# Optimization experiments

Hardware: AMD Instinct MI355X
Metric: run time of the kernel (lower is better)

Reference implementation:

```python
import jax, jax.numpy as jnp
import numpy as np

N_NODES = 50000
N_EDGES = 800000
D = 64


def setup_inputs() -> dict:
    key = jax.random.key(0)
    ks = jax.random.split(key, 8)
    feats = jax.random.normal(ks[0], (N_NODES, D), dtype=jnp.float32)
    src = jax.random.randint(ks[1], (N_EDGES,), 0, N_NODES, dtype=jnp.int32)
    dst = jax.random.randint(ks[2], (N_EDGES,), 0, N_NODES, dtype=jnp.int32)
    s = 1.0 / np.sqrt(D)
    return {
        "features": feats,
        "src": src,
        "dst": dst,
        "W_self1": jax.random.normal(ks[3], (D, D), dtype=jnp.float32) * s,
        "W_neigh1": jax.random.normal(ks[4], (D, D), dtype=jnp.float32) * s,
        "b1": jnp.zeros((D,), dtype=jnp.float32),
        "W_self2": jax.random.normal(ks[5], (D, D), dtype=jnp.float32) * s,
        "W_neigh2": jax.random.normal(ks[6], (D, D), dtype=jnp.float32) * s,
        "b2": jnp.zeros((D,), dtype=jnp.float32),
    }


def _sage_mean(feat, src, dst, W_self, W_neigh, b):
    # mean-aggregate neighbor features: sum over incoming edges / clamp(in_deg, 1)
    msg_sum = jax.ops.segment_sum(feat[src], dst, num_segments=N_NODES)
    deg = jax.ops.segment_sum(jnp.ones(src.shape, feat.dtype), dst, num_segments=N_NODES)
    h_neigh = msg_sum / jnp.maximum(deg, 1.0)[:, None]
    return feat @ W_self + h_neigh @ W_neigh + b


def reference(features, src, dst, W_self1, W_neigh1, b1, W_self2, W_neigh2, b2):
    x = jax.nn.relu(_sage_mean(features, src, dst, W_self1, W_neigh1, b1))
    x = jax.nn.relu(_sage_mean(x, src, dst, W_self2, W_neigh2, b2))
    # DotProductPredictor: u_dot_v per edge, sigmoid; forward applies sigmoid again
    edge_dot = jnp.sum(x[src] * x[dst], axis=-1)  # [E]
    return jax.nn.sigmoid(jax.nn.sigmoid(edge_dot))
```

## Files before the change

kernel.cpp:

```cpp
#include <hip/hip_runtime.h>
#include <math.h>

#define N_NODES 50000
#define N_EDGES 800000
#define D 64
#define CAP 48
#define NPART 8
#define PART_N (N_NODES / NPART)
#define ACHUNK 2048
#define NBLK_A ((N_EDGES + ACHUNK - 1) / ACHUNK)
#define SEG_CAP 448
#define NB_PER_PART 32

#define FB_OFF   0
#define HB_OFF   6400000
#define STG_OFF  12800000
#define CNTG_OFF 18432000
#define POS_OFF  19200000
#define BKT_OFF  19400704

__device__ __forceinline__ unsigned int bf_rtn(float x) {
    unsigned int b = __float_as_uint(x);
    return (b + 0x7fffu + ((b >> 16) & 1u)) >> 16;
}
__device__ __forceinline__ unsigned int bf2_pack(float lo, float hi) {
    return bf_rtn(lo) | (bf_rtn(hi) << 16);
}
__device__ __forceinline__ float4 bf4_unpack(uint2 q) {
    float4 r;
    r.x = __uint_as_float(q.x << 16);
    r.y = __uint_as_float(q.x & 0xffff0000u);
    r.z = __uint_as_float(q.y << 16);
    r.w = __uint_as_float(q.y & 0xffff0000u);
    return r;
}

__global__ void convert_feats_kernel(const float4* __restrict__ in, uint2* __restrict__ out,
                                     int* __restrict__ pos) {
    int i = blockIdx.x * blockDim.x + threadIdx.x;
    if (i < N_NODES) pos[i] = 0;
    float4 v = in[i];
    uint2 q;
    q.x = bf2_pack(v.x, v.y);
    q.y = bf2_pack(v.z, v.w);
    out[i] = q;
}

__global__ __launch_bounds__(256) void partition_edges_kernel(
    const int* __restrict__ src, const int* __restrict__ dst,
    unsigned int* __restrict__ stage, int* __restrict__ cntg) {
    __shared__ int cnt[NPART];
    const int tid = threadIdx.x;
    if (tid < NPART) cnt[tid] = 0;
    __syncthreads();

    const int base = blockIdx.x * ACHUNK;
    unsigned int* bstage = stage + blockIdx.x * (NPART * SEG_CAP);
#pragma unroll
    for (int j = 0; j < ACHUNK / 256; ++j) {
        int i = base + j * 256 + tid;
        if (i < N_EDGES) {
            int d = dst[i];
            int s = src[i];
            int p = d / PART_N;
            unsigned int val = ((unsigned int)(d - p * PART_N) << 16) | (unsigned int)s;
            int slot = atomicAdd(&cnt[p], 1);
            if (slot < SEG_CAP) bstage[p * SEG_CAP + slot] = val;
        }
    }
    __syncthreads();
    if (tid < NPART) cntg[blockIdx.x * NPART + tid] = cnt[tid];
}

__global__ __launch_bounds__(256) void scatter_bucket_kernel(
    const unsigned int* __restrict__ stage, const int* __restrict__ cntg,
    int* __restrict__ pos, int* __restrict__ bucket) {
    const int p = blockIdx.x & (NPART - 1);
    const int j = blockIdx.x >> 3;
    const int lo = p * PART_N;
    const int tid = threadIdx.x;
    for (int b = j; b < NBLK_A; b += NB_PER_PART) {
        const int c = cntg[b * NPART + p];
        const unsigned int* seg = stage + (b * NPART + p) * SEG_CAP;
        for (int i = tid; i < c; i += 256) {
            unsigned int v = seg[i];
            int d = lo + (int)(v >> 16);
            int s = (int)(v & 0xffffu);
            int slot = atomicAdd(&pos[d], 1);
            if (slot < CAP) bucket[d * CAP + slot] = s;
        }
    }
}

__global__ __launch_bounds__(256) void gather_mean_kernel(
    const uint2* __restrict__ xb,
    const int* __restrict__ pos,
    const int* __restrict__ bucket,
    uint2* __restrict__ h_out) {
    const int tid = threadIdx.x;
    const int lane = tid & 63;
    const int g = lane >> 4;
    const int sub = lane & 15;
    const int node = blockIdx.x * 16 + (tid >> 6) * 4 + g;

    const int deg = pos[node];
    const int cnt = (deg < CAP) ? deg : CAP;
    const int* brow = bucket + node * CAP;

#define ACC4(A, R) { A.x += R.x; A.y += R.y; A.z += R.z; A.w += R.w; }
    float4 a0 = make_float4(0.f, 0.f, 0.f, 0.f);
    float4 a1 = make_float4(0.f, 0.f, 0.f, 0.f);
    float4 a2 = make_float4(0.f, 0.f, 0.f, 0.f);
    float4 a3 = make_float4(0.f, 0.f, 0.f, 0.f);
    float4 a4 = make_float4(0.f, 0.f, 0.f, 0.f);
    float4 a5 = make_float4(0.f, 0.f, 0.f, 0.f);
    float4 a6 = make_float4(0.f, 0.f, 0.f, 0.f);
    float4 a7 = make_float4(0.f, 0.f, 0.f, 0.f);
    int j = 0;
    for (; j + 8 <= cnt; j += 8) {
        int4 i0 = *(const int4*)(brow + j);
        int4 i1 = *(const int4*)(brow + j + 4);
        float4 r0 = bf4_unpack(xb[i0.x * 16 + sub]);
        float4 r1 = bf4_unpack(xb[i0.y * 16 + sub]);
        float4 r2 = bf4_unpack(xb[i0.z * 16 + sub]);
        float4 r3 = bf4_unpack(xb[i0.w * 16 + sub]);
        float4 r4 = bf4_unpack(xb[i1.x * 16 + sub]);
        float4 r5 = bf4_unpack(xb[i1.y * 16 + sub]);
        float4 r6 = bf4_unpack(xb[i1.z * 16 + sub]);
        float4 r7 = bf4_unpack(xb[i1.w * 16 + sub]);
        ACC4(a0, r0); ACC4(a1, r1); ACC4(a2, r2); ACC4(a3, r3);
        ACC4(a4, r4); ACC4(a5, r5); ACC4(a6, r6); ACC4(a7, r7);
    }
    if (j + 4 <= cnt) {
        int4 i0 = *(const int4*)(brow + j);
        float4 r0 = bf4_unpack(xb[i0.x * 16 + sub]);
        float4 r1 = bf4_unpack(xb[i0.y * 16 + sub]);
        float4 r2 = bf4_unpack(xb[i0.z * 16 + sub]);
        float4 r3 = bf4_unpack(xb[i0.w * 16 + sub]);
        ACC4(a4, r0); ACC4(a5, r1); ACC4(a6, r2); ACC4(a7, r3);
        j += 4;
    }
    for (; j < cnt; ++j) {
        float4 r = bf4_unpack(xb[brow[j] * 16 + sub]);
        ACC4(a0, r);
    }
#undef ACC4
    float4 acc;
    acc.x = ((a0.x + a1.x) + (a2.x + a3.x)) + ((a4.x + a5.x) + (a6.x + a7.x));
    acc.y = ((a0.y + a1.y) + (a2.y + a3.y)) + ((a4.y + a5.y) + (a6.y + a7.y));
    acc.z = ((a0.z + a1.z) + (a2.z + a3.z)) + ((a4.z + a5.z) + (a6.z + a7.z));
    acc.w = ((a0.w + a1.w) + (a2.w + a3.w)) + ((a4.w + a5.w) + (a6.w + a7.w));
    float inv = 1.0f / fmaxf((float)deg, 1.0f);
    uint2 q;
    q.x = bf2_pack(acc.x * inv, acc.y * inv);
    q.y = bf2_pack(acc.z * inv, acc.w * inv);
    h_out[node * 16 + sub] = q;
}

__global__ __launch_bounds__(64, 3) void sage_gemm_kernel(
    const uint2* xb_self,
    const uint2* hb_in,
    const float* __restrict__ W_self, const float* __restrict__ W_neigh,
    const float* __restrict__ bias,
    uint2* x_out) {
    const int lane = threadIdx.x;
    const int g = lane >> 4;
    const int sub = lane & 15;
    const int nb = blockIdx.x * 16;

    const int n0 = nb + 0 * 4 + g;
    const int n1 = nb + 1 * 4 + g;
    const int n2 = nb + 2 * 4 + g;
    const int n3 = nb + 3 * 4 + g;
    const uint2* arow0 = xb_self + n0 * 16;
    const uint2* arow1 = xb_self + n1 * 16;
    const uint2* arow2 = xb_self + n2 * 16;
    const uint2* arow3 = xb_self + n3 * 16;
    const uint2* hrow0 = hb_in + n0 * 16;
    const uint2* hrow1 = hb_in + n1 * 16;
    const uint2* hrow2 = hb_in + n2 * 16;
    const uint2* hrow3 = hb_in + n3 * 16;

    const float4* Wsg = (const float4*)W_self;
    const float4* Wng = (const float4*)W_neigh;
    const float4 b4 = ((const float4*)bias)[sub];
    float4 accs0 = b4, accs1 = b4, accs2 = b4, accs3 = b4;

#pragma unroll 4
    for (int kk = 0; kk < 16; ++kk) {
        float4 ws0 = Wsg[(kk * 4 + 0) * 16 + sub];
        float4 ws1 = Wsg[(kk * 4 + 1) * 16 + sub];
        float4 ws2 = Wsg[(kk * 4 + 2) * 16 + sub];
        float4 ws3 = Wsg[(kk * 4 + 3) * 16 + sub];
        float4 wn0 = Wng[(kk * 4 + 0) * 16 + sub];
        float4 wn1 = Wng[(kk * 4 + 1) * 16 + sub];
        float4 wn2 = Wng[(kk * 4 + 2) * 16 + sub];
        float4 wn3 = Wng[(kk * 4 + 3) * 16 + sub];

#define SAGE_FMA(ACC, AROW, HROW)                                               \
        {                                                                       \
            float4 a4 = bf4_unpack((AROW)[kk]);                                 \
            float4 h4v = bf4_unpack((HROW)[kk]);                                \
            ACC.x += a4.x * ws0.x + a4.y * ws1.x + a4.z * ws2.x + a4.w * ws3.x  \
                   + h4v.x * wn0.x + h4v.y * wn1.x + h4v.z * wn2.x + h4v.w * wn3.x; \
            ACC.y += a4.x * ws0.y + a4.y * ws1.y + a4.z * ws2.y + a4.w * ws3.y  \
                   + h4v.x * wn0.y + h4v.y * wn1.y + h4v.z * wn2.y + h4v.w * wn3.y; \
            ACC.z += a4.x * ws0.z + a4.y * ws1.z + a4.z * ws2.z + a4.w * ws3.z  \
                   + h4v.x * wn0.z + h4v.y * wn1.z + h4v.z * wn2.z + h4v.w * wn3.z; \
            ACC.w += a4.x * ws0.w + a4.y * ws1.w + a4.z * ws2.w + a4.w * ws3.w  \
                   + h4v.x * wn0.w + h4v.y * wn1.w + h4v.z * wn2.w + h4v.w * wn3.w; \
        }
        SAGE_FMA(accs0, arow0, hrow0);
        SAGE_FMA(accs1, arow1, hrow1);
        SAGE_FMA(accs2, arow2, hrow2);
        SAGE_FMA(accs3, arow3, hrow3);
#undef SAGE_FMA
    }

#define SAGE_STORE(N, ACC)                                                      \
    {                                                                           \
        float rx = fmaxf(ACC.x, 0.f), ry = fmaxf(ACC.y, 0.f);                   \
        float rz = fmaxf(ACC.z, 0.f), rw = fmaxf(ACC.w, 0.f);                   \
        uint2 q; q.x = bf2_pack(rx, ry); q.y = bf2_pack(rz, rw);                \
        x_out[(N) * 16 + sub] = q;                                              \
    }
    SAGE_STORE(n0, accs0);
    SAGE_STORE(n1, accs1);
    SAGE_STORE(n2, accs2);
    SAGE_STORE(n3, accs3);
#undef SAGE_STORE
}

__global__ __launch_bounds__(256) void edge_dot_kernel(
    const uint2* __restrict__ xb,
    const int* __restrict__ src,
    const int* __restrict__ dst,
    float* __restrict__ out) {
    const int tid = threadIdx.x;
    const int grp = tid >> 4;
    const int sub = tid & 15;
    const int e0 = (blockIdx.x * 16 + grp) * 8;

    int4 sa = *(const int4*)(src + e0);
    int4 sb = *(const int4*)(src + e0 + 4);
    int4 da = *(const int4*)(dst + e0);
    int4 db = *(const int4*)(dst + e0 + 4);

    float4 as0 = bf4_unpack(xb[sa.x * 16 + sub]);
    float4 ad0 = bf4_unpack(xb[da.x * 16 + sub]);
    float4 as1 = bf4_unpack(xb[sa.y * 16 + sub]);
    float4 ad1 = bf4_unpack(xb[da.y * 16 + sub]);
    float4 as2 = bf4_unpack(xb[sa.z * 16 + sub]);
    float4 ad2 = bf4_unpack(xb[da.z * 16 + sub]);
    float4 as3 = bf4_unpack(xb[sa.w * 16 + sub]);
    float4 ad3 = bf4_unpack(xb[da.w * 16 + sub]);
    float4 as4 = bf4_unpack(xb[sb.x * 16 + sub]);
    float4 ad4 = bf4_unpack(xb[db.x * 16 + sub]);
    float4 as5 = bf4_unpack(xb[sb.y * 16 + sub]);
    float4 ad5 = bf4_unpack(xb[db.y * 16 + sub]);
    float4 as6 = bf4_unpack(xb[sb.z * 16 + sub]);
    float4 ad6 = bf4_unpack(xb[db.z * 16 + sub]);
    float4 as7 = bf4_unpack(xb[sb.w * 16 + sub]);
    float4 ad7 = bf4_unpack(xb[db.w * 16 + sub]);

#define EDGE_EMIT(U, AS, AD)                                                    \
    {                                                                           \
        float p = (AS).x * (AD).x + (AS).y * (AD).y                             \
                + (AS).z * (AD).z + (AS).w * (AD).w;                            \
        p += __shfl_xor(p, 1);                                                  \
        p += __shfl_xor(p, 2);                                                  \
        p += __shfl_xor(p, 4);                                                  \
        p += __shfl_xor(p, 8);                                                  \
        if (sub == 0) {                                                         \
            float s1v = 1.f / (1.f + __expf(-p));                               \
            out[e0 + (U)] = 1.f / (1.f + __expf(-s1v));                         \
        }                                                                       \
    }
    EDGE_EMIT(0, as0, ad0);
    EDGE_EMIT(1, as1, ad1);
    EDGE_EMIT(2, as2, ad2);
    EDGE_EMIT(3, as3, ad3);
    EDGE_EMIT(4, as4, ad4);
    EDGE_EMIT(5, as5, ad5);
    EDGE_EMIT(6, as6, ad6);
    EDGE_EMIT(7, as7, ad7);
#undef EDGE_EMIT
}

extern "C" void kernel_launch(void* const* d_in, const int* in_sizes, int n_in,
                              void* d_out, int out_size, void* d_ws, size_t ws_size,
                              hipStream_t stream) {
    const float* feats = (const float*)d_in[0];
    const int* src = (const int*)d_in[1];
    const int* dst = (const int*)d_in[2];
    const float* Ws1 = (const float*)d_in[3];
    const float* Wn1 = (const float*)d_in[4];
    const float* b1 = (const float*)d_in[5];
    const float* Ws2 = (const float*)d_in[6];
    const float* Wn2 = (const float*)d_in[7];
    const float* b2 = (const float*)d_in[8];
    float* out = (float*)d_out;

    char* ws = (char*)d_ws;
    uint2* fb            = (uint2*)(ws + FB_OFF);
    uint2* hb            = (uint2*)(ws + HB_OFF);
    unsigned int* stage  = (unsigned int*)(ws + STG_OFF);
    int* cntg            = (int*)(ws + CNTG_OFF);
    int* pos             = (int*)(ws + POS_OFF);
    int* bucket          = (int*)(ws + BKT_OFF);

    convert_feats_kernel<<<(N_NODES * 16) / 256, 256, 0, stream>>>((const float4*)feats, fb, pos);
    partition_edges_kernel<<<NBLK_A, 256, 0, stream>>>(src, dst, stage, cntg);
    scatter_bucket_kernel<<<NPART * NB_PER_PART, 256, 0, stream>>>(stage, cntg, pos, bucket);

    const int gather_grid = N_NODES / 16;
    const int gemm_grid = N_NODES / 16;

    gather_mean_kernel<<<gather_grid, 256, 0, stream>>>(fb, pos, bucket, hb);
    sage_gemm_kernel<<<gemm_grid, 64, 0, stream>>>(fb, hb, Ws1, Wn1, b1, fb);
    gather_mean_kernel<<<gather_grid, 256, 0, stream>>>(fb, pos, bucket, hb);
    sage_gemm_kernel<<<gemm_grid, 64, 0, stream>>>(fb, hb, Ws2, Wn2, b2, hb);

    edge_dot_kernel<<<N_EDGES / 128, 256, 0, stream>>>((const uint2*)hb, src, dst, out);
}
```

Measured before the change: 166.7 us.

## Fuse gather-mean with SAGE GEMM per layer and merge prep kernels

Merges the feature conversion and edge partition kernels into one launch split by block index. Fuses the neighbor mean gather with the per-node dense transform, so the aggregated vector stays in shared memory instead of round-tripping through a bf16 buffer in global memory. Each thread now computes one node's output slice rather than four, and the buffers ping-pong between fb and hb. This drops two launches and the intermediate writes and reads, at the cost of higher register pressure and weight loads repeated across more threads.

Measured after the change: 201.9 us. +21.1%, slower.

```diff
diff --git a/kernel.cpp b/kernel.cpp
--- a/kernel.cpp
+++ b/kernel.cpp
@@ -11,6 +11,7 @@
 #define NBLK_A ((N_EDGES + ACHUNK - 1) / ACHUNK)
 #define SEG_CAP 448
 #define NB_PER_PART 32
+#define CONV_BLKS 3125
 
 #define FB_OFF   0
 #define HB_OFF   6400000
@@ -35,41 +36,41 @@
     return r;
 }
 
-__global__ void convert_feats_kernel(const float4* __restrict__ in, uint2* __restrict__ out,
-                                     int* __restrict__ pos) {
-    int i = blockIdx.x * blockDim.x + threadIdx.x;
-    if (i < N_NODES) pos[i] = 0;
-    float4 v = in[i];
-    uint2 q;
-    q.x = bf2_pack(v.x, v.y);
-    q.y = bf2_pack(v.z, v.w);
-    out[i] = q;
-}
-
-__global__ __launch_bounds__(256) void partition_edges_kernel(
+__global__ __launch_bounds__(256) void prep_kernel(
+    const float4* __restrict__ feats, uint2* __restrict__ fb, int* __restrict__ pos,
     const int* __restrict__ src, const int* __restrict__ dst,
     unsigned int* __restrict__ stage, int* __restrict__ cntg) {
-    __shared__ int cnt[NPART];
-    const int tid = threadIdx.x;
-    if (tid < NPART) cnt[tid] = 0;
-    __syncthreads();
-
-    const int base = blockIdx.x * ACHUNK;
-    unsigned int* bstage = stage + blockIdx.x * (NPART * SEG_CAP);
+    const int tid = threadIdx.x;
+    if (blockIdx.x < CONV_BLKS) {
+        int i = blockIdx.x * 256 + tid;
+        if (i < N_NODES) pos[i] = 0;
+        float4 v = feats[i];
+        uint2 q;
+        q.x = bf2_pack(v.x, v.y);
+        q.y = bf2_pack(v.z, v.w);
+        fb[i] = q;
+    } else {
+        const int pb = blockIdx.x - CONV_BLKS;
+        __shared__ int cnt[NPART];
+        if (tid < NPART) cnt[tid] = 0;
+        __syncthreads();
+        const int base = pb * ACHUNK;
+        unsigned int* bstage = stage + pb * (NPART * SEG_CAP);
 #pragma unroll
-    for (int j = 0; j < ACHUNK / 256; ++j) {
-        int i = base + j * 256 + tid;
-        if (i < N_EDGES) {
-            int d = dst[i];
-            int s = src[i];
-            int p = d / PART_N;
-            unsigned int val = ((unsigned int)(d - p * PART_N) << 16) | (unsigned int)s;
-            int slot = atomicAdd(&cnt[p], 1);
-            if (slot < SEG_CAP) bstage[p * SEG_CAP + slot] = val;
+        for (int j = 0; j < ACHUNK / 256; ++j) {
+            int i = base + j * 256 + tid;
+            if (i < N_EDGES) {
+                int d = dst[i];
+                int s = src[i];
+                int p = d / PART_N;
+                unsigned int val = ((unsigned int)(d - p * PART_N) << 16) | (unsigned int)s;
+                int slot = atomicAdd(&cnt[p], 1);
+                if (slot < SEG_CAP) bstage[p * SEG_CAP + slot] = val;
+            }
         }
-    }
-    __syncthreads();
-    if (tid < NPART) cntg[blockIdx.x * NPART + tid] = cnt[tid];
+        __syncthreads();
+        if (tid < NPART) cntg[pb * NPART + tid] = cnt[tid];
+    }
 }
 
 __global__ __launch_bounds__(256) void scatter_bucket_kernel(
@@ -92,16 +93,21 @@
     }
 }
 
-__global__ __launch_bounds__(256) void gather_mean_kernel(
-    const uint2* __restrict__ xb,
+__global__ __launch_bounds__(256) void sage_layer_kernel(
+    const uint2* __restrict__ xb_in,
     const int* __restrict__ pos,
     const int* __restrict__ bucket,
-    uint2* __restrict__ h_out) {
-    const int tid = threadIdx.x;
+    const float* __restrict__ W_self, const float* __restrict__ W_neigh,
+    const float* __restrict__ bias,
+    uint2* __restrict__ x_out) {
+    __shared__ float4 hL[4][4][17];
+
+    const int tid = threadIdx.x;
+    const int w = tid >> 6;
     const int lane = tid & 63;
     const int g = lane >> 4;
     const int sub = lane & 15;
-    const int node = blockIdx.x * 16 + (tid >> 6) * 4 + g;
+    const int node = blockIdx.x * 16 + w * 4 + g;
 
     const int deg = pos[node];
     const int cnt = (deg < CAP) ? deg : CAP;
@@ -120,71 +126,45 @@
     for (; j + 8 <= cnt; j += 8) {
         int4 i0 = *(const int4*)(brow + j);
         int4 i1 = *(const int4*)(brow + j + 4);
-        float4 r0 = bf4_unpack(xb[i0.x * 16 + sub]);
-        float4 r1 = bf4_unpack(xb[i0.y * 16 + sub]);
-        float4 r2 = bf4_unpack(xb[i0.z * 16 + sub]);
-        float4 r3 = bf4_unpack(xb[i0.w * 16 + sub]);
-        float4 r4 = bf4_unpack(xb[i1.x * 16 + sub]);
-        float4 r5 = bf4_unpack(xb[i1.y * 16 + sub]);
-        float4 r6 = bf4_unpack(xb[i1.z * 16 + sub]);
-        float4 r7 = bf4_unpack(xb[i1.w * 16 + sub]);
+        float4 r0 = bf4_unpack(xb_in[i0.x * 16 + sub]);
+        float4 r1 = bf4_unpack(xb_in[i0.y * 16 + sub]);
+        float4 r2 = bf4_unpack(xb_in[i0.z * 16 + sub]);
+        float4 r3 = bf4_unpack(xb_in[i0.w * 16 + sub]);
+        float4 r4 = bf4_unpack(xb_in[i1.x * 16 + sub]);
+        float4 r5 = bf4_unpack(xb_in[i1.y * 16 + sub]);
+        float4 r6 = bf4_unpack(xb_in[i1.z * 16 + sub]);
+        float4 r7 = bf4_unpack(xb_in[i1.w * 16 + sub]);
         ACC4(a0, r0); ACC4(a1, r1); ACC4(a2, r2); ACC4(a3, r3);
         ACC4(a4, r4); ACC4(a5, r5); ACC4(a6, r6); ACC4(a7, r7);
     }
     if (j + 4 <= cnt) {
         int4 i0 = *(const int4*)(brow + j);
-        float4 r0 = bf4_unpack(xb[i0.x * 16 + sub]);
-        float4 r1 = bf4_unpack(xb[i0.y * 16 + sub]);
-        float4 r2 = bf4_unpack(xb[i0.z * 16 + sub]);
-        float4 r3 = bf4_unpack(xb[i0.w * 16 + sub]);
+        float4 r0 = bf4_unpack(xb_in[i0.x * 16 + sub]);
+        float4 r1 = bf4_unpack(xb_in[i0.y * 16 + sub]);
+        float4 r2 = bf4_unpack(xb_in[i0.z * 16 + sub]);
+        float4 r3 = bf4_unpack(xb_in[i0.w * 16 + sub]);
         ACC4(a4, r0); ACC4(a5, r1); ACC4(a6, r2); ACC4(a7, r3);
         j += 4;
     }
     for (; j < cnt; ++j) {
-        float4 r = bf4_unpack(xb[brow[j] * 16 + sub]);
+        float4 r = bf4_unpack(xb_in[brow[j] * 16 + sub]);
         ACC4(a0, r);
     }
 #undef ACC4
-    float4 acc;
-    acc.x = ((a0.x + a1.x) + (a2.x + a3.x)) + ((a4.x + a5.x) + (a6.x + a7.x));
-    acc.y = ((a0.y + a1.y) + (a2.y + a3.y)) + ((a4.y + a5.y) + (a6.y + a7.y));
-    acc.z = ((a0.z + a1.z) + (a2.z + a3.z)) + ((a4.z + a5.z) + (a6.z + a7.z));
-    acc.w = ((a0.w + a1.w) + (a2.w + a3.w)) + ((a4.w + a5.w) + (a6.w + a7.w));
+    float4 hv;
+    hv.x = ((a0.x + a1.x) + (a2.x + a3.x)) + ((a4.x + a5.x) + (a6.x + a7.x));
+    hv.y = ((a0.y + a1.y) + (a2.y + a3.y)) + ((a4.y + a5.y) + (a6.y + a7.y));
+    hv.z = ((a0.z + a1.z) + (a2.z + a3.z)) + ((a4.z + a5.z) + (a6.z + a7.z));
+    hv.w = ((a0.w + a1.w) + (a2.w + a3.w)) + ((a4.w + a5.w) + (a6.w + a7.w));
     float inv = 1.0f / fmaxf((float)deg, 1.0f);
-    uint2 q;
-    q.x = bf2_pack(acc.x * inv, acc.y * inv);
-    q.y = bf2_pack(acc.z * inv, acc.w * inv);
-    h_out[node * 16 + sub] = q;
-}
-
-__global__ __launch_bounds__(64, 3) void sage_gemm_kernel(
-    const uint2* xb_self,
-    const uint2* hb_in,
-    const float* __restrict__ W_self, const float* __restrict__ W_neigh,
-    const float* __restrict__ bias,
-    uint2* x_out) {
-    const int lane = threadIdx.x;
-    const int g = lane >> 4;
-    const int sub = lane & 15;
-    const int nb = blockIdx.x * 16;
-
-    const int n0 = nb + 0 * 4 + g;
-    const int n1 = nb + 1 * 4 + g;
-    const int n2 = nb + 2 * 4 + g;
-    const int n3 = nb + 3 * 4 + g;
-    const uint2* arow0 = xb_self + n0 * 16;
-    const uint2* arow1 = xb_self + n1 * 16;
-    const uint2* arow2 = xb_self + n2 * 16;
-    const uint2* arow3 = xb_self + n3 * 16;
-    const uint2* hrow0 = hb_in + n0 * 16;
-    const uint2* hrow1 = hb_in + n1 * 16;
-    const uint2* hrow2 = hb_in + n2 * 16;
-    const uint2* hrow3 = hb_in + n3 * 16;
-
+    hv.x *= inv; hv.y *= inv; hv.z *= inv; hv.w *= inv;
+    hL[w][g][sub] = hv;
+
+    const uint2* arow = xb_in + node * 16;
+    const float4* hrow = &hL[w][g][0];
     const float4* Wsg = (const float4*)W_self;
     const float4* Wng = (const float4*)W_neigh;
-    const float4 b4 = ((const float4*)bias)[sub];
-    float4 accs0 = b4, accs1 = b4, accs2 = b4, accs3 = b4;
+    float4 acc = ((const float4*)bias)[sub];
 
 #pragma unroll 4
     for (int kk = 0; kk < 16; ++kk) {
@@ -196,39 +176,24 @@
         float4 wn1 = Wng[(kk * 4 + 1) * 16 + sub];
         float4 wn2 = Wng[(kk * 4 + 2) * 16 + sub];
         float4 wn3 = Wng[(kk * 4 + 3) * 16 + sub];
-
-#define SAGE_FMA(ACC, AROW, HROW)                                               \
-        {                                                                       \
-            float4 a4 = bf4_unpack((AROW)[kk]);                                 \
-            float4 h4v = bf4_unpack((HROW)[kk]);                                \
-            ACC.x += a4.x * ws0.x + a4.y * ws1.x + a4.z * ws2.x + a4.w * ws3.x  \
-                   + h4v.x * wn0.x + h4v.y * wn1.x + h4v.z * wn2.x + h4v.w * wn3.x; \
-            ACC.y += a4.x * ws0.y + a4.y * ws1.y + a4.z * ws2.y + a4.w * ws3.y  \
-                   + h4v.x * wn0.y + h4v.y * wn1.y + h4v.z * wn2.y + h4v.w * wn3.y; \
-            ACC.z += a4.x * ws0.z + a4.y * ws1.z + a4.z * ws2.z + a4.w * ws3.z  \
-                   + h4v.x * wn0.z + h4v.y * wn1.z + h4v.z * wn2.z + h4v.w * wn3.z; \
-            ACC.w += a4.x * ws0.w + a4.y * ws1.w + a4.z * ws2.w + a4.w * ws3.w  \
-                   + h4v.x * wn0.w + h4v.y * wn1.w + h4v.z * wn2.w + h4v.w * wn3.w; \
-        }
-        SAGE_FMA(accs0, arow0, hrow0);
-        SAGE_FMA(accs1, arow1, hrow1);
-        SAGE_FMA(accs2, arow2, hrow2);
-        SAGE_FMA(accs3, arow3, hrow3);
-#undef SAGE_FMA
-    }
-
-#define SAGE_STORE(N, ACC)                                                      \
-    {                                                                           \
-        float rx = fmaxf(ACC.x, 0.f), ry = fmaxf(ACC.y, 0.f);                   \
-        float rz = fmaxf(ACC.z, 0.f), rw = fmaxf(ACC.w, 0.f);                   \
-        uint2 q; q.x = bf2_pack(rx, ry); q.y = bf2_pack(rz, rw);                \
-        x_out[(N) * 16 + sub] = q;                                              \
-    }
-    SAGE_STORE(n0, accs0);
-    SAGE_STORE(n1, accs1);
-    SAGE_STORE(n2, accs2);
-    SAGE_STORE(n3, accs3);
-#undef SAGE_STORE
+        float4 av = bf4_unpack(arow[kk]);
+        float4 h4 = hrow[kk];
+        acc.x += av.x * ws0.x + av.y * ws1.x + av.z * ws2.x + av.w * ws3.x
+               + h4.x * wn0.x + h4.y * wn1.x + h4.z * wn2.x + h4.w * wn3.x;
+        acc.y += av.x * ws0.y + av.y * ws1.y + av.z * ws2.y + av.w * ws3.y
+               + h4.x * wn0.y + h4.y * wn1.y + h4.z * wn2.y + h4.w * wn3.y;
+        acc.z += av.x * ws0.z + av.y * ws1.z + av.z * ws2.z + av.w * ws3.z
+               + h4.x * wn0.z + h4.y * wn1.z + h4.z * wn2.z + h4.w * wn3.z;
+        acc.w += av.x * ws0.w + av.y * ws1.w + av.z * ws2.w + av.w * ws3.w
+               + h4.x * wn0.w + h4.y * wn1.w + h4.z * wn2.w + h4.w * wn3.w;
+    }
+
+    float rx = fmaxf(acc.x, 0.f), ry = fmaxf(acc.y, 0.f);
+    float rz = fmaxf(acc.z, 0.f), rw = fmaxf(acc.w, 0.f);
+    uint2 q;
+    q.x = bf2_pack(rx, ry);
+    q.y = bf2_pack(rz, rw);
+    x_out[node * 16 + sub] = q;
 }
 
 __global__ __launch_bounds__(256) void edge_dot_kernel(
@@ -309,17 +274,14 @@
     int* pos             = (int*)(ws + POS_OFF);
     int* bucket          = (int*)(ws + BKT_OFF);
 
-    convert_feats_kernel<<<(N_NODES * 16) / 256, 256, 0, stream>>>((const float4*)feats, fb, pos);
-    partition_edges_kernel<<<NBLK_A, 256, 0, stream>>>(src, dst, stage, cntg);
+    prep_kernel<<<CONV_BLKS + NBLK_A, 256, 0, stream>>>(
+        (const float4*)feats, fb, pos, src, dst, stage, cntg);
     scatter_bucket_kernel<<<NPART * NB_PER_PART, 256, 0, stream>>>(stage, cntg, pos, bucket);
 
-    const int gather_grid = N_NODES / 16;
-    const int gemm_grid = N_NODES / 16;
-
-    gather_mean_kernel<<<gather_grid, 256, 0, stream>>>(fb, pos, bucket, hb);
-    sage_gemm_kernel<<<gemm_grid, 64, 0, stream>>>(fb, hb, Ws1, Wn1, b1, fb);
-    gather_mean_kernel<<<gather_grid, 256, 0, stream>>>(fb, pos, bucket, hb);
-    sage_gemm_kernel<<<gemm_grid, 64, 0, stream>>>(fb, hb, Ws2, Wn2, b2, hb);
-
-    edge_dot_kernel<<<N_EDGES / 128, 256, 0, stream>>>((const uint2*)hb, src, dst, out);
-}
+    const int layer_grid = N_NODES / 16;
+
+    sage_layer_kernel<<<layer_grid, 256, 0, stream>>>(fb, pos, bucket, Ws1, Wn1, b1, hb);
+    sage_layer_kernel<<<layer_grid, 256, 0, stream>>>(hb, pos, bucket, Ws2, Wn2, b2, fb);
+
+    edge_dot_kernel<<<N_EDGES / 128, 256, 0, stream>>>((const uint2*)fb, src, dst, out);
+}
```
